# Kernel tuning notes

Measured on AMD Instinct MI355X. Metric: run time of the kernel, lower is better.

Reference implementation:

```python
import jax, jax.numpy as jnp
import numpy as np

B, S, D, H = 8, 2048, 256, 4
HD = D // H  # 64
EPS = 1e-5


def setup_inputs() -> dict:
    key = jax.random.key(0)
    ks = jax.random.split(key, 16)
    sc = 0.05
    return {
        "descriptors": jax.random.normal(ks[0], (B, S, D), jnp.float32),
        "source": jax.random.normal(ks[1], (B, S, D), jnp.float32),
        "mask": jnp.ones((B, S), jnp.int32),
        # attention projections (stored as [in, out])
        "q_w": jax.random.normal(ks[2], (D, D), jnp.float32) * sc,
        "q_b": jnp.zeros((D,), jnp.float32),
        "k_w": jax.random.normal(ks[3], (D, D), jnp.float32) * sc,
        "k_b": jnp.zeros((D,), jnp.float32),
        "v_w": jax.random.normal(ks[4], (D, D), jnp.float32) * sc,
        "v_b": jnp.zeros((D,), jnp.float32),
        "o_w": jax.random.normal(ks[5], (D, D), jnp.float32) * sc,
        "o_b": jnp.zeros((D,), jnp.float32),
        # MLP layer 0: 2D -> 2D, BatchNorm1d (eval mode) + ReLU
        "m0_w": jax.random.normal(ks[6], (2 * D, 2 * D), jnp.float32) * sc,
        "m0_b": jnp.zeros((2 * D,), jnp.float32),
        "bn_g": jax.random.uniform(ks[7], (2 * D,), jnp.float32, 0.5, 1.5),
        "bn_b": jax.random.normal(ks[8], (2 * D,), jnp.float32) * 0.1,
        "bn_m": jax.random.normal(ks[9], (2 * D,), jnp.float32) * 0.1,
        "bn_v": jax.random.uniform(ks[10], (2 * D,), jnp.float32, 0.5, 1.5),
        # MLP layer 1: 2D -> D, no activation
        "m1_w": jax.random.normal(ks[11], (2 * D, D), jnp.float32) * sc,
        "m1_b": jnp.zeros((D,), jnp.float32),
    }


def reference(descriptors, source, mask, q_w, q_b, k_w, k_b, v_w, v_b, o_w, o_b,
              m0_w, m0_b, bn_g, bn_b, bn_m, bn_v, m1_w, m1_b):
    # Multi-head cross-attention: query=descriptors, key=value=source
    q = (descriptors @ q_w + q_b).reshape(B, S, H, HD).transpose(0, 2, 1, 3)  # [B,H,S,HD]
    k = (source @ k_w + k_b).reshape(B, S, H, HD).transpose(0, 2, 1, 3)
    v = (source @ v_w + v_b).reshape(B, S, H, HD).transpose(0, 2, 1, 3)

    scores = jnp.einsum("bhqd,bhkd->bhqk", q, k) / jnp.sqrt(jnp.float32(HD))
    scores = jnp.where(mask[:, None, None, :] == 0, -1e9, scores)
    probs = jax.nn.softmax(scores.astype(jnp.float32), axis=-1)  # [B,H,S,S]

    ctx = jnp.einsum("bhqk,bhkd->bhqd", probs, v)  # [B,H,S,HD]
    ctx = ctx.transpose(0, 2, 1, 3).reshape(B, S, D)
    attn_out = ctx @ o_w + o_b  # out_proj

    # concat + MLP (Linear -> BatchNorm1d(eval) -> ReLU -> Linear)
    h = jnp.concatenate([descriptors, attn_out], axis=-1)  # [B,S,2D]
    h = h @ m0_w + m0_b
    h = (h - bn_m) * jax.lax.rsqrt(bn_v + EPS) * bn_g + bn_b  # per-channel BN
    h = jax.nn.relu(h)
    h = h @ m1_w + m1_b  # [B,S,D]
    return h
```

## Files before the change

kernel.cpp:

```cpp
#include <hip/hip_runtime.h>

#define NB 8
#define NS 2048
#define ND 256
#define NH 4
#define NHD 64
#define ND2 512
#define NM (NB * NS)
#define PITCH 72
#define C1 0.18033688f

typedef __attribute__((ext_vector_type(8))) short          bf16x8;
typedef __attribute__((ext_vector_type(4))) float          f32x4;
typedef unsigned short ushort_t;
typedef unsigned int   uint_t;

#define MFMA16(a, b, c) __builtin_amdgcn_mfma_f32_16x16x32_bf16(a, b, c, 0, 0, 0)

#if __has_builtin(__builtin_amdgcn_exp2f)
#define EXP2(x) __builtin_amdgcn_exp2f(x)
#else
#define EXP2(x) exp2f(x)
#endif

static __device__ inline uint_t pack2bf(float a, float b) {
    union { float f; uint_t u; } x, y; x.f = a; y.f = b;
    return __builtin_amdgcn_perm(y.u + 0x8000u, x.u + 0x8000u, 0x07060302u);
}
static __device__ inline ushort_t f2bf(float f) {
    union { float f; uint_t u; } x; x.f = f;
    return (ushort_t)((x.u + 0x7FFFu + ((x.u >> 16) & 1u)) >> 16);
}


__global__ __launch_bounds__(256) void conv_frag(
    const float* __restrict__ d, const float* __restrict__ s,
    ushort_t* __restrict__ df, ushort_t* __restrict__ sf)
{
    const float* src = blockIdx.y ? s : d;
    ushort_t* dst    = blockIdx.y ? sf : df;
    const int g = blockIdx.x * 256 + threadIdx.x;
    const int lane = g & 63, ci = g >> 6;
    const int kc = ci & 7, r16 = ci >> 3;
    const int row = r16 * 16 + (lane & 15);
    const int c0  = kc * 32 + (lane >> 4) * 8;
    const float* p = src + (size_t)row * ND + c0;
    float4 a = *(const float4*)p;
    float4 b = *(const float4*)(p + 4);
    uint4 pk;
    pk.x = pack2bf(a.x, a.y); pk.y = pack2bf(a.z, a.w);
    pk.z = pack2bf(b.x, b.y); pk.w = pack2bf(b.z, b.w);
    *(uint4*)(dst + (size_t)g * 8) = pk;
}

__global__ __launch_bounds__(256) void wfrag(
    const float* q, const float* k, const float* v, const float* m1,
    ushort_t* qw, ushort_t* kw, ushort_t* vw, ushort_t* m1f)
{
    const float* src; ushort_t* dst; int K, N; float sc = 1.0f;
    switch (blockIdx.y) {
        case 0: src = q;  dst = qw;  K = 256; N = 256; sc = C1; break;
        case 1: src = k;  dst = kw;  K = 256; N = 256; break;
        case 2: src = v;  dst = vw;  K = 256; N = 256; break;
        default: src = m1; dst = m1f; K = 512; N = 256; break;
    }
    const int g = blockIdx.x * 256 + threadIdx.x;
    if (g >= (N * K) / 8) return;
    const int lane = g & 63, ci = g >> 6;
    const int lgck = (K == 512) ? 4 : 3;
    const int kc = ci & ((1 << lgck) - 1), n16 = ci >> lgck;
    const int n  = n16 * 16 + (lane & 15);
    const int k0 = kc * 32 + (lane >> 4) * 8;
    float f[8];
#pragma unroll
    for (int j = 0; j < 8; j++) f[j] = src[(size_t)(k0 + j) * N + n] * sc;
    uint4 pk;
    pk.x = pack2bf(f[0], f[1]); pk.y = pack2bf(f[2], f[3]);
    pk.z = pack2bf(f[4], f[5]); pk.w = pack2bf(f[6], f[7]);
    *(uint4*)(dst + (size_t)g * 8) = pk;
}

static __device__ inline void femit(ushort_t* buf, int n, int k, float v) {
    const int kc = k >> 5;
    const int lane = (((k >> 3) & 3) << 4) | (n & 15);
    const int j = k & 7;
    buf[((size_t)(((n >> 4) * 16 + kc) * 64 + lane)) * 8 + j] = f2bf(v);
}

__global__ __launch_bounds__(256) void fuse_w(
    const float* __restrict__ o_w, const float* __restrict__ o_b,
    const float* __restrict__ m0_w, const float* __restrict__ m0_b,
    const float* __restrict__ bng, const float* __restrict__ bnb,
    const float* __restrict__ bnm, const float* __restrict__ bnv,
    ushort_t* __restrict__ m0fF, float* __restrict__ biasf)
{
    __shared__ float red[256];
    const int n = blockIdx.x;
    const int i = threadIdx.x;
    const float A = bng[n] * rsqrtf(bnv[n] + 1e-5f);
    float f = 0.f;
#pragma unroll 8
    for (int j = 0; j < 256; j++)
        f += o_w[i * 256 + j] * m0_w[(size_t)(256 + j) * 512 + n];
    femit(m0fF, n, 256 + i, f * A);
    femit(m0fF, n, i, m0_w[(size_t)i * 512 + n] * A);
    red[i] = o_b[i] * m0_w[(size_t)(256 + i) * 512 + n];
    __syncthreads();
    for (int s = 128; s > 0; s >>= 1) {
        if (i < s) red[i] += red[i + s];
        __syncthreads();
    }
    if (i == 0) biasf[n] = (m0_b[n] + red[0] - bnm[n]) * A + bnb[n];
}

__global__ __launch_bounds__(256) void make_mbias(
    const int* __restrict__ mask, float* __restrict__ mb)
{
    const int i = blockIdx.x * 256 + threadIdx.x;
    mb[i] = mask[i] ? 0.0f : -1e9f;
}

template <int KC, int AK, bool NAT>
static __device__ inline void core4(
    const ushort_t* __restrict__ A0, const ushort_t* __restrict__ A1,
    const ushort_t* __restrict__ WF, int t16, int n16, f32x4 acc[4][4])
{
    const int lane = threadIdx.x & 63;
#pragma unroll
    for (int kc = 0; kc < KC; kc++) {
        const ushort_t* Ab = (kc < AK) ? A0 : A1;
        const int kca = (kc < AK) ? kc : kc - AK;
        bf16x8 af[4], wf[4];
#pragma unroll
        for (int mt = 0; mt < 4; mt++)
            af[mt] = *(const bf16x8*)(Ab + ((size_t)((t16 + mt) * AK + kca) * 64 + lane) * 8);
#pragma unroll
        for (int nt = 0; nt < 4; nt++)
            wf[nt] = *(const bf16x8*)(WF + ((size_t)((n16 + nt) * KC + kc) * 64 + lane) * 8);
#pragma unroll
        for (int mt = 0; mt < 4; mt++)
#pragma unroll
            for (int nt = 0; nt < 4; nt++) {
                if (NAT) acc[mt][nt] = MFMA16(af[mt], wf[nt], acc[mt][nt]);
                else     acc[mt][nt] = MFMA16(wf[nt], af[mt], acc[mt][nt]);
            }
    }
}

__global__ __launch_bounds__(256) void qkv_frag(
    const ushort_t* __restrict__ descF, const ushort_t* __restrict__ srcF,
    const ushort_t* __restrict__ qwF, const ushort_t* __restrict__ kwF,
    const ushort_t* __restrict__ vwF,
    const float* __restrict__ q_b, const float* __restrict__ k_b,
    const float* __restrict__ v_b,
    ushort_t* __restrict__ qF, ushort_t* __restrict__ kF,
    ushort_t* __restrict__ vF)
{
    const int t = threadIdx.x, w = t >> 6;
    const int lq = t & 15, lg = (t & 63) >> 4;
    const int h    = blockIdx.x;
    const int tok0 = (blockIdx.y << 8) + (w << 6);
    const int t16  = tok0 >> 4, n16 = h << 2;
    const int z    = blockIdx.z;

    f32x4 acc[4][4];
#pragma unroll
    for (int mt = 0; mt < 4; mt++)
#pragma unroll
        for (int nt = 0; nt < 4; nt++) acc[mt][nt] = (f32x4){0.f, 0.f, 0.f, 0.f};

    if (z == 2) {
        core4<8, 8, true>(srcF, srcF, vwF, t16, n16, acc);
#pragma unroll
        for (int nt = 0; nt < 4; nt++) {
            const int dvh = nt * 16 + lq;
            const float bs = v_b[h * 64 + dvh];
#pragma unroll
            for (int mt = 0; mt < 4; mt++) {
                const int tok = tok0 + mt * 16 + lg * 4;
                const int b = tok >> 11, s0 = tok & 2047;
                const int bh = b * NH + h;
                uint2 pv;
                pv.x = pack2bf(acc[mt][nt][0] + bs, acc[mt][nt][1] + bs);
                pv.y = pack2bf(acc[mt][nt][2] + bs, acc[mt][nt][3] + bs);
                const size_t e = (size_t)bh * 131072 +
                    ((size_t)((dvh >> 4) * 64 + (s0 >> 5)) * 64 +
                     (((s0 >> 3) & 3) * 16 + (dvh & 15))) * 8 + (s0 & 7);
                *(uint2*)(vF + e) = pv;
            }
        }
    } else {
        const ushort_t* A = z ? srcF : descF;
        const ushort_t* W = z ? kwF : qwF;
        const float* bias = z ? k_b : q_b;
        ushort_t* dst     = z ? kF : qF;
        const float bsc   = z ? 1.0f : C1;
        core4<8, 8, false>(A, A, W, t16, n16, acc);
#pragma unroll
        for (int nt = 0; nt < 4; nt++) {
            const int d0 = nt * 16 + lg * 4;
            f32x4 b4 = *(const f32x4*)(bias + h * 64 + d0);
#pragma unroll
            for (int mt = 0; mt < 4; mt++) {
                const int tok = tok0 + mt * 16 + lq;
                const int b = tok >> 11, s = tok & 2047;
                const int bh = b * NH + h;
                uint2 pv;
                pv.x = pack2bf(acc[mt][nt][0] + b4[0] * bsc,
                               acc[mt][nt][1] + b4[1] * bsc);
                pv.y = pack2bf(acc[mt][nt][2] + b4[2] * bsc,
                               acc[mt][nt][3] + b4[3] * bsc);
                const size_t e = (size_t)bh * 131072 +
                    ((size_t)((s >> 4) * 2 + (d0 >> 5)) * 64 +
                     (((d0 >> 3) & 3) * 16 + lq)) * 8 + (d0 & 7);
                *(uint2*)(dst + e) = pv;
            }
        }
    }
}

__global__ __launch_bounds__(256) void mlp0_frag(
    const ushort_t* __restrict__ descF, const ushort_t* __restrict__ ctxF,
    const ushort_t* __restrict__ m0fF, const float* __restrict__ biasf,
    ushort_t* __restrict__ hF)
{
    const int t = threadIdx.x, w = t >> 6;
    const int lq = t & 15, lg = (t & 63) >> 4;
    const int n0   = blockIdx.x << 6;
    const int tok0 = (blockIdx.y << 8) + (w << 6);
    const int t16  = tok0 >> 4, n16 = n0 >> 4;

    f32x4 acc[4][4];
#pragma unroll
    for (int mt = 0; mt < 4; mt++)
#pragma unroll
        for (int nt = 0; nt < 4; nt++) acc[mt][nt] = (f32x4){0.f, 0.f, 0.f, 0.f};

    core4<16, 8, false>(descF, ctxF, m0fF, t16, n16, acc);

#pragma unroll
    for (int nt = 0; nt < 4; nt++) {
        const int c0 = n0 + nt * 16 + lg * 4;
        f32x4 b4 = *(const f32x4*)(biasf + c0);
#pragma unroll
        for (int mt = 0; mt < 4; mt++) {
            const int tok = tok0 + mt * 16 + lq;
            uint2 pv;
            pv.x = pack2bf(fmaxf(acc[mt][nt][0] + b4[0], 0.f),
                           fmaxf(acc[mt][nt][1] + b4[1], 0.f));
            pv.y = pack2bf(fmaxf(acc[mt][nt][2] + b4[2], 0.f),
                           fmaxf(acc[mt][nt][3] + b4[3], 0.f));
            const size_t e = ((size_t)((tok >> 4) * 16 + (c0 >> 5)) * 64 +
                              (((c0 >> 3) & 3) * 16 + lq)) * 8 + (c0 & 7);
            *(uint2*)(hF + e) = pv;
        }
    }
}

__global__ __launch_bounds__(256) void mlp1_frag(
    const ushort_t* __restrict__ hF, const ushort_t* __restrict__ m1F,
    const float* __restrict__ m1_b, float* __restrict__ out)
{
    const int t = threadIdx.x, w = t >> 6;
    const int lq = t & 15, lg = (t & 63) >> 4;
    const int n0   = blockIdx.x << 6;
    const int tok0 = (blockIdx.y << 8) + (w << 6);
    const int t16  = tok0 >> 4, n16 = n0 >> 4;

    f32x4 acc[4][4];
#pragma unroll
    for (int mt = 0; mt < 4; mt++)
#pragma unroll
        for (int nt = 0; nt < 4; nt++) acc[mt][nt] = (f32x4){0.f, 0.f, 0.f, 0.f};

    core4<16, 16, false>(hF, hF, m1F, t16, n16, acc);

#pragma unroll
    for (int nt = 0; nt < 4; nt++) {
        const int c0 = n0 + nt * 16 + lg * 4;
        f32x4 b4 = *(const f32x4*)(m1_b + c0);
#pragma unroll
        for (int mt = 0; mt < 4; mt++) {
            const int tok = tok0 + mt * 16 + lq;
            f32x4 o4;
#pragma unroll
            for (int j = 0; j < 4; j++) o4[j] = acc[mt][nt][j] + b4[j];
            *(f32x4*)(out + (size_t)tok * ND + c0) = o4;
        }
    }
}

__global__ __launch_bounds__(256) void attn_frag(
    const ushort_t* __restrict__ qF, const ushort_t* __restrict__ kF,
    const ushort_t* __restrict__ vF, const float* __restrict__ mbias,
    ushort_t* __restrict__ ctxF)
{
    __shared__ ushort_t Pl[8][16 * PITCH];

    const int t = threadIdx.x, w = t >> 6, lane = t & 63;
    const int lq = t & 15, lg = lane >> 4;
    const int qb = blockIdx.x, h = blockIdx.y, b = blockIdx.z;
    const int bh = b * NH + h;

    const ushort_t* qh = qF + (size_t)bh * 131072;
    const ushort_t* kh = kF + (size_t)bh * 131072;
    const ushort_t* vh = vF + (size_t)bh * 131072;
    const float* mrow = mbias + b * NS;
    const int qrow0 = qb * 128 + w * 32;
    const int q16 = qrow0 >> 4;

    bf16x8 qf[2][2];
#pragma unroll
    for (int qt = 0; qt < 2; qt++)
#pragma unroll
        for (int kc = 0; kc < 2; kc++)
            qf[qt][kc] = *(const bf16x8*)(qh + ((size_t)((q16 + qt) * 2 + kc) * 64 + lane) * 8);

    f32x4 o[2][4];
#pragma unroll
    for (int qt = 0; qt < 2; qt++)
#pragma unroll
        for (int dt = 0; dt < 4; dt++) o[qt][dt] = (f32x4){0.f, 0.f, 0.f, 0.f};
    float l_part[2] = {0.0f, 0.0f};

    bf16x8 ka[4][2];
#pragma unroll
    for (int kt = 0; kt < 4; kt++)
#pragma unroll
        for (int kk = 0; kk < 2; kk++)
            ka[kt][kk] = *(const bf16x8*)(kh + ((size_t)((kt * 2 + kk) * 64 + lane)) * 8);

    for (int key0 = 0; key0 < NS; key0 += 64) {
        bf16x8 vf[4][2];
        const ushort_t* vb = vh + (size_t)(key0 >> 5) * 512;
#pragma unroll
        for (int dt = 0; dt < 4; dt++)
#pragma unroll
            for (int kh2 = 0; kh2 < 2; kh2++)
                vf[dt][kh2] = *(const bf16x8*)(vb +
                    ((size_t)((dt * 64 + kh2) * 64 + lane)) * 8);
        f32x4 mb[4];
#pragma unroll
        for (int kt = 0; kt < 4; kt++)
            mb[kt] = *(const f32x4*)(mrow + key0 + kt * 16 + lg * 4);

        f32x4 st[2][4];
#pragma unroll
        for (int qt = 0; qt < 2; qt++)
#pragma unroll
            for (int kt = 0; kt < 4; kt++) {
                f32x4 a = (f32x4){0.f, 0.f, 0.f, 0.f};
                a = MFMA16(ka[kt][0], qf[qt][0], a);
                a = MFMA16(ka[kt][1], qf[qt][1], a);
                st[qt][kt] = a;
            }

        const int keyn = (key0 + 64) & (NS - 1);
        const ushort_t* kb = kh + (size_t)keyn * 64;
        bf16x8 kn[4][2];
#pragma unroll
        for (int kt = 0; kt < 4; kt++)
#pragma unroll
            for (int kk = 0; kk < 2; kk++)
                kn[kt][kk] = *(const bf16x8*)(kb + ((size_t)((kt * 2 + kk) * 64 + lane)) * 8);

#pragma unroll
        for (int qt = 0; qt < 2; qt++) {
            float ls = 0.0f;
#pragma unroll
            for (int kt = 0; kt < 4; kt++) {
                float pr[4];
#pragma unroll
                for (int r = 0; r < 4; r++) {
                    const float p = EXP2(st[qt][kt][r] + mb[kt][r]);
                    ls += p;
                    pr[r] = p;
                }
                uint2 pv;
                pv.x = pack2bf(pr[0], pr[1]);
                pv.y = pack2bf(pr[2], pr[3]);
                *(uint2*)&Pl[w * 2 + qt][lq * PITCH + kt * 16 + lg * 4] = pv;
            }
            l_part[qt] += ls;
        }

        bf16x8 pf[2][2];
#pragma unroll
        for (int qt = 0; qt < 2; qt++)
#pragma unroll
            for (int kh2 = 0; kh2 < 2; kh2++)
                pf[qt][kh2] = *(const bf16x8*)&Pl[w * 2 + qt][lq * PITCH + kh2 * 32 + lg * 8];

#pragma unroll
        for (int dt = 0; dt < 4; dt++)
#pragma unroll
            for (int kh2 = 0; kh2 < 2; kh2++)
#pragma unroll
                for (int qt = 0; qt < 2; qt++)
                    o[qt][dt] = MFMA16(vf[dt][kh2], pf[qt][kh2], o[qt][dt]);

#pragma unroll
        for (int kt = 0; kt < 4; kt++)
#pragma unroll
            for (int kk = 0; kk < 2; kk++)
                ka[kt][kk] = kn[kt][kk];
    }

#pragma unroll
    for (int qt = 0; qt < 2; qt++) {
        float ls = l_part[qt];
        ls += __shfl_xor(ls, 16);
        ls += __shfl_xor(ls, 32);
        const float li = 1.0f / ls;
        const int tok16 = b * 128 + q16 + qt;
#pragma unroll
        for (int dt = 0; dt < 4; dt++) {
            const int c = h * 64 + dt * 16 + lg * 4;
            uint2 pv;
            pv.x = pack2bf(o[qt][dt][0] * li, o[qt][dt][1] * li);
            pv.y = pack2bf(o[qt][dt][2] * li, o[qt][dt][3] * li);
            const size_t e = ((size_t)(tok16 * 8 + (c >> 5)) * 64 +
                              (((c >> 3) & 3) * 16 + lq)) * 8 + (c & 7);
            *(uint2*)(ctxF + e) = pv;
        }
    }
}

extern "C" void kernel_launch(void* const* d_in, const int* in_sizes, int n_in,
                              void* d_out, int out_size, void* d_ws, size_t ws_size,
                              hipStream_t stream)
{
    (void)in_sizes; (void)n_in; (void)out_size; (void)ws_size;
    const float* desc = (const float*)d_in[0];
    const float* srcp = (const float*)d_in[1];
    const int*   mask = (const int*)d_in[2];
    const float* q_w  = (const float*)d_in[3];
    const float* q_b  = (const float*)d_in[4];
    const float* k_w  = (const float*)d_in[5];
    const float* k_b  = (const float*)d_in[6];
    const float* v_w  = (const float*)d_in[7];
    const float* v_b  = (const float*)d_in[8];
    const float* o_w  = (const float*)d_in[9];
    const float* o_b  = (const float*)d_in[10];
    const float* m0_w = (const float*)d_in[11];
    const float* m0_b = (const float*)d_in[12];
    const float* bng  = (const float*)d_in[13];
    const float* bnb  = (const float*)d_in[14];
    const float* bnm  = (const float*)d_in[15];
    const float* bnv  = (const float*)d_in[16];
    const float* m1_w = (const float*)d_in[17];
    const float* m1_b = (const float*)d_in[18];
    float* out = (float*)d_out;

    const size_t ASZ = (size_t)NM * ND;
    ushort_t* descF = (ushort_t*)d_ws;
    ushort_t* srcF  = descF + ASZ;
    ushort_t* qF    = descF + 2 * ASZ;
    ushort_t* kF    = descF + 3 * ASZ;
    ushort_t* vF    = descF + 4 * ASZ;
    ushort_t* qwF   = descF + 5 * ASZ;
    ushort_t* kwF   = qwF + 65536;
    ushort_t* vwF   = kwF + 65536;
    ushort_t* m1F   = vwF + 65536;
    ushort_t* m0fF  = m1F + 131072;
    float*    biasf = (float*)(m0fF + 262144);
    float*    mbias = biasf + 512;
    ushort_t* ctxF  = srcF;
    ushort_t* hF    = qF;

    const dim3 blk(256);

    conv_frag<<<dim3(2048, 2), blk, 0, stream>>>(desc, srcp, descF, srcF);
    wfrag<<<dim3(64, 4), blk, 0, stream>>>(q_w, k_w, v_w, m1_w, qwF, kwF, vwF, m1F);
    fuse_w<<<dim3(512), blk, 0, stream>>>(o_w, o_b, m0_w, m0_b,
                                          bng, bnb, bnm, bnv, m0fF, biasf);
    make_mbias<<<dim3(64), blk, 0, stream>>>(mask, mbias);

    qkv_frag<<<dim3(4, NM / 256, 3), blk, 0, stream>>>(
        descF, srcF, qwF, kwF, vwF, q_b, k_b, v_b, qF, kF, vF);
    attn_frag<<<dim3(NS / 128, NH, NB), blk, 0, stream>>>(qF, kF, vF, mbias, ctxF);
    mlp0_frag<<<dim3(8, NM / 256), blk, 0, stream>>>(descF, ctxF, m0fF, biasf, hF);
    mlp1_frag<<<dim3(4, NM / 256), blk, 0, stream>>>(hF, m1F, m1_b, out);
}
```

Before: 245.2 us.

## Restructure weight fusion, double-buffer GEMM fragments, halve attention block size

```diff
diff --git a/kernel.cpp b/kernel.cpp
--- a/kernel.cpp
+++ b/kernel.cpp
@@ -88,29 +88,44 @@
 }
 
 __global__ __launch_bounds__(256) void fuse_w(
-    const float* __restrict__ o_w, const float* __restrict__ o_b,
-    const float* __restrict__ m0_w, const float* __restrict__ m0_b,
+    const float* __restrict__ o_w, const float* __restrict__ m0_w,
+    const float* __restrict__ bng, const float* __restrict__ bnv,
+    ushort_t* __restrict__ m0fF)
+{
+    __shared__ float ow[256];
+    const int i = blockIdx.x;
+    const int t = threadIdx.x;
+    ow[t] = o_w[i * 256 + t];
+    __syncthreads();
+    float f0 = 0.f, f1 = 0.f;
+#pragma unroll 4
+    for (int j = 0; j < 256; j++) {
+        const float w = ow[j];
+        f0 += w * m0_w[(size_t)(256 + j) * 512 + t];
+        f1 += w * m0_w[(size_t)(256 + j) * 512 + t + 256];
+    }
+    const float A0v = bng[t] * rsqrtf(bnv[t] + 1e-5f);
+    const float A1v = bng[t + 256] * rsqrtf(bnv[t + 256] + 1e-5f);
+    femit(m0fF, t, 256 + i, f0 * A0v);
+    femit(m0fF, t + 256, 256 + i, f1 * A1v);
+    femit(m0fF, t, i, m0_w[(size_t)i * 512 + t] * A0v);
+    femit(m0fF, t + 256, i, m0_w[(size_t)i * 512 + t + 256] * A1v);
+}
+
+__global__ __launch_bounds__(256) void bias_f(
+    const float* __restrict__ o_b, const float* __restrict__ m0_w,
+    const float* __restrict__ m0_b,
     const float* __restrict__ bng, const float* __restrict__ bnb,
     const float* __restrict__ bnm, const float* __restrict__ bnv,
-    ushort_t* __restrict__ m0fF, float* __restrict__ biasf)
-{
-    __shared__ float red[256];
-    const int n = blockIdx.x;
-    const int i = threadIdx.x;
+    float* __restrict__ biasf)
+{
+    const int n = blockIdx.x * 256 + threadIdx.x;
+    float s = 0.f;
+#pragma unroll 4
+    for (int j = 0; j < 256; j++)
+        s += o_b[j] * m0_w[(size_t)(256 + j) * 512 + n];
     const float A = bng[n] * rsqrtf(bnv[n] + 1e-5f);
-    float f = 0.f;
-#pragma unroll 8
-    for (int j = 0; j < 256; j++)
-        f += o_w[i * 256 + j] * m0_w[(size_t)(256 + j) * 512 + n];
-    femit(m0fF, n, 256 + i, f * A);
-    femit(m0fF, n, i, m0_w[(size_t)i * 512 + n] * A);
-    red[i] = o_b[i] * m0_w[(size_t)(256 + i) * 512 + n];
-    __syncthreads();
-    for (int s = 128; s > 0; s >>= 1) {
-        if (i < s) red[i] += red[i + s];
-        __syncthreads();
-    }
-    if (i == 0) biasf[n] = (m0_b[n] + red[0] - bnm[n]) * A + bnb[n];
+    biasf[n] = (m0_b[n] + s - bnm[n]) * A + bnb[n];
 }
 
 __global__ __launch_bounds__(256) void make_mbias(
@@ -126,23 +141,33 @@
     const ushort_t* __restrict__ WF, int t16, int n16, f32x4 acc[4][4])
 {
     const int lane = threadIdx.x & 63;
+    bf16x8 af[2][4], wf[2][4];
+#pragma unroll
+    for (int mt = 0; mt < 4; mt++)
+        af[0][mt] = *(const bf16x8*)(A0 + ((size_t)((t16 + mt) * AK) * 64 + lane) * 8);
+#pragma unroll
+    for (int nt = 0; nt < 4; nt++)
+        wf[0][nt] = *(const bf16x8*)(WF + ((size_t)((n16 + nt) * KC) * 64 + lane) * 8);
 #pragma unroll
     for (int kc = 0; kc < KC; kc++) {
-        const ushort_t* Ab = (kc < AK) ? A0 : A1;
-        const int kca = (kc < AK) ? kc : kc - AK;
-        bf16x8 af[4], wf[4];
+        const int cur = kc & 1, nxt = cur ^ 1;
+        if (kc + 1 < KC) {
+            const int kn = kc + 1;
+            const ushort_t* Ab = (kn < AK) ? A0 : A1;
+            const int kca = (kn < AK) ? kn : kn - AK;
+#pragma unroll
+            for (int mt = 0; mt < 4; mt++)
+                af[nxt][mt] = *(const bf16x8*)(Ab + ((size_t)((t16 + mt) * AK + kca) * 64 + lane) * 8);
+#pragma unroll
+            for (int nt = 0; nt < 4; nt++)
+                wf[nxt][nt] = *(const bf16x8*)(WF + ((size_t)((n16 + nt) * KC + kn) * 64 + lane) * 8);
+        }
 #pragma unroll
         for (int mt = 0; mt < 4; mt++)
-            af[mt] = *(const bf16x8*)(Ab + ((size_t)((t16 + mt) * AK + kca) * 64 + lane) * 8);
-#pragma unroll
-        for (int nt = 0; nt < 4; nt++)
-            wf[nt] = *(const bf16x8*)(WF + ((size_t)((n16 + nt) * KC + kc) * 64 + lane) * 8);
-#pragma unroll
-        for (int mt = 0; mt < 4; mt++)
 #pragma unroll
             for (int nt = 0; nt < 4; nt++) {
-                if (NAT) acc[mt][nt] = MFMA16(af[mt], wf[nt], acc[mt][nt]);
-                else     acc[mt][nt] = MFMA16(wf[nt], af[mt], acc[mt][nt]);
+                if (NAT) acc[mt][nt] = MFMA16(af[cur][mt], wf[cur][nt], acc[mt][nt]);
+                else     acc[mt][nt] = MFMA16(wf[cur][nt], af[cur][mt], acc[mt][nt]);
             }
     }
 }
@@ -290,12 +315,12 @@
     }
 }
 
-__global__ __launch_bounds__(256) void attn_frag(
+__global__ __launch_bounds__(128) void attn_frag(
     const ushort_t* __restrict__ qF, const ushort_t* __restrict__ kF,
     const ushort_t* __restrict__ vF, const float* __restrict__ mbias,
     ushort_t* __restrict__ ctxF)
 {
-    __shared__ ushort_t Pl[8][16 * PITCH];
+    __shared__ ushort_t Pl[4][16 * PITCH];
 
     const int t = threadIdx.x, w = t >> 6, lane = t & 63;
     const int lq = t & 15, lg = lane >> 4;
@@ -306,7 +331,7 @@
     const ushort_t* kh = kF + (size_t)bh * 131072;
     const ushort_t* vh = vF + (size_t)bh * 131072;
     const float* mrow = mbias + b * NS;
-    const int qrow0 = qb * 128 + w * 32;
+    const int qrow0 = qb * 64 + w * 32;
     const int q16 = qrow0 >> 4;
 
     bf16x8 qf[2][2];
@@ -472,13 +497,13 @@
 
     conv_frag<<<dim3(2048, 2), blk, 0, stream>>>(desc, srcp, descF, srcF);
     wfrag<<<dim3(64, 4), blk, 0, stream>>>(q_w, k_w, v_w, m1_w, qwF, kwF, vwF, m1F);
-    fuse_w<<<dim3(512), blk, 0, stream>>>(o_w, o_b, m0_w, m0_b,
-                                          bng, bnb, bnm, bnv, m0fF, biasf);
+    fuse_w<<<dim3(256), blk, 0, stream>>>(o_w, m0_w, bng, bnv, m0fF);
+    bias_f<<<dim3(2), blk, 0, stream>>>(o_b, m0_w, m0_b, bng, bnb, bnm, bnv, biasf);
     make_mbias<<<dim3(64), blk, 0, stream>>>(mask, mbias);
 
     qkv_frag<<<dim3(4, NM / 256, 3), blk, 0, stream>>>(
         descF, srcF, qwF, kwF, vwF, q_b, k_b, v_b, qF, kF, vF);
-    attn_frag<<<dim3(NS / 128, NH, NB), blk, 0, stream>>>(qF, kF, vF, mbias, ctxF);
+    attn_frag<<<dim3(NS / 64, NH, NB), dim3(128), 0, stream>>>(qF, kF, vF, mbias, ctxF);
     mlp0_frag<<<dim3(8, NM / 256), blk, 0, stream>>>(descF, ctxF, m0fF, biasf, hF);
     mlp1_frag<<<dim3(4, NM / 256), blk, 0, stream>>>(hF, m1F, m1_b, out);
 }
```

New measurement: 269.3 us. +9.8%, slower.

## Merge prep kernels, restructure fuse_w, remap attention blocks, shrink mlp1 tiles

Applied to the files above, without the earlier changes.

```diff
diff --git a/kernel.cpp b/kernel.cpp
--- a/kernel.cpp
+++ b/kernel.cpp
@@ -33,53 +33,6 @@
 }
 
 
-__global__ __launch_bounds__(256) void conv_frag(
-    const float* __restrict__ d, const float* __restrict__ s,
-    ushort_t* __restrict__ df, ushort_t* __restrict__ sf)
-{
-    const float* src = blockIdx.y ? s : d;
-    ushort_t* dst    = blockIdx.y ? sf : df;
-    const int g = blockIdx.x * 256 + threadIdx.x;
-    const int lane = g & 63, ci = g >> 6;
-    const int kc = ci & 7, r16 = ci >> 3;
-    const int row = r16 * 16 + (lane & 15);
-    const int c0  = kc * 32 + (lane >> 4) * 8;
-    const float* p = src + (size_t)row * ND + c0;
-    float4 a = *(const float4*)p;
-    float4 b = *(const float4*)(p + 4);
-    uint4 pk;
-    pk.x = pack2bf(a.x, a.y); pk.y = pack2bf(a.z, a.w);
-    pk.z = pack2bf(b.x, b.y); pk.w = pack2bf(b.z, b.w);
-    *(uint4*)(dst + (size_t)g * 8) = pk;
-}
-
-__global__ __launch_bounds__(256) void wfrag(
-    const float* q, const float* k, const float* v, const float* m1,
-    ushort_t* qw, ushort_t* kw, ushort_t* vw, ushort_t* m1f)
-{
-    const float* src; ushort_t* dst; int K, N; float sc = 1.0f;
-    switch (blockIdx.y) {
-        case 0: src = q;  dst = qw;  K = 256; N = 256; sc = C1; break;
-        case 1: src = k;  dst = kw;  K = 256; N = 256; break;
-        case 2: src = v;  dst = vw;  K = 256; N = 256; break;
-        default: src = m1; dst = m1f; K = 512; N = 256; break;
-    }
-    const int g = blockIdx.x * 256 + threadIdx.x;
-    if (g >= (N * K) / 8) return;
-    const int lane = g & 63, ci = g >> 6;
-    const int lgck = (K == 512) ? 4 : 3;
-    const int kc = ci & ((1 << lgck) - 1), n16 = ci >> lgck;
-    const int n  = n16 * 16 + (lane & 15);
-    const int k0 = kc * 32 + (lane >> 4) * 8;
-    float f[8];
-#pragma unroll
-    for (int j = 0; j < 8; j++) f[j] = src[(size_t)(k0 + j) * N + n] * sc;
-    uint4 pk;
-    pk.x = pack2bf(f[0], f[1]); pk.y = pack2bf(f[2], f[3]);
-    pk.z = pack2bf(f[4], f[5]); pk.w = pack2bf(f[6], f[7]);
-    *(uint4*)(dst + (size_t)g * 8) = pk;
-}
-
 static __device__ inline void femit(ushort_t* buf, int n, int k, float v) {
     const int kc = k >> 5;
     const int lane = (((k >> 3) & 3) << 4) | (n & 15);
@@ -87,58 +40,122 @@
     buf[((size_t)(((n >> 4) * 16 + kc) * 64 + lane)) * 8 + j] = f2bf(v);
 }
 
-__global__ __launch_bounds__(256) void fuse_w(
+__global__ __launch_bounds__(256) void prep(
+    const float* __restrict__ desc, const float* __restrict__ srcp,
+    const int* __restrict__ mask,
+    const float* __restrict__ q_w, const float* __restrict__ k_w,
+    const float* __restrict__ v_w, const float* __restrict__ m1_w,
     const float* __restrict__ o_w, const float* __restrict__ o_b,
     const float* __restrict__ m0_w, const float* __restrict__ m0_b,
     const float* __restrict__ bng, const float* __restrict__ bnb,
     const float* __restrict__ bnm, const float* __restrict__ bnv,
-    ushort_t* __restrict__ m0fF, float* __restrict__ biasf)
-{
-    __shared__ float red[256];
-    const int n = blockIdx.x;
-    const int i = threadIdx.x;
-    const float A = bng[n] * rsqrtf(bnv[n] + 1e-5f);
-    float f = 0.f;
-#pragma unroll 8
-    for (int j = 0; j < 256; j++)
-        f += o_w[i * 256 + j] * m0_w[(size_t)(256 + j) * 512 + n];
-    femit(m0fF, n, 256 + i, f * A);
-    femit(m0fF, n, i, m0_w[(size_t)i * 512 + n] * A);
-    red[i] = o_b[i] * m0_w[(size_t)(256 + i) * 512 + n];
-    __syncthreads();
-    for (int s = 128; s > 0; s >>= 1) {
-        if (i < s) red[i] += red[i + s];
+    ushort_t* __restrict__ descF, ushort_t* __restrict__ srcF,
+    ushort_t* __restrict__ qwF, ushort_t* __restrict__ kwF,
+    ushort_t* __restrict__ vwF, ushort_t* __restrict__ m1F,
+    ushort_t* __restrict__ m0fF, float* __restrict__ biasf,
+    float* __restrict__ mbias)
+{
+    __shared__ float ow[256];
+    const int blk = blockIdx.x;
+    const int t = threadIdx.x;
+
+    if (blk < 4096) {
+        const int y = blk >> 11, x = blk & 2047;
+        const float* src = y ? srcp : desc;
+        ushort_t* dst    = y ? srcF : descF;
+        const int g = x * 256 + t;
+        const int lane = g & 63, ci = g >> 6;
+        const int kc = ci & 7, r16 = ci >> 3;
+        const int row = r16 * 16 + (lane & 15);
+        const int c0  = kc * 32 + (lane >> 4) * 8;
+        const float* p = src + (size_t)row * ND + c0;
+        float4 a = *(const float4*)p;
+        float4 b = *(const float4*)(p + 4);
+        uint4 pk;
+        pk.x = pack2bf(a.x, a.y); pk.y = pack2bf(a.z, a.w);
+        pk.z = pack2bf(b.x, b.y); pk.w = pack2bf(b.z, b.w);
+        *(uint4*)(dst + (size_t)g * 8) = pk;
+    } else if (blk < 4352) {
+        const int wb = blk - 4096;
+        const int y = wb >> 6, x = wb & 63;
+        const float* src; ushort_t* dst; int K, N; float sc = 1.0f;
+        switch (y) {
+            case 0: src = q_w; dst = qwF; K = 256; N = 256; sc = C1; break;
+            case 1: src = k_w; dst = kwF; K = 256; N = 256; break;
+            case 2: src = v_w; dst = vwF; K = 256; N = 256; break;
+            default: src = m1_w; dst = m1F; K = 512; N = 256; break;
+        }
+        const int g = x * 256 + t;
+        if (g >= (N * K) / 8) return;
+        const int lane = g & 63, ci = g >> 6;
+        const int lgck = (K == 512) ? 4 : 3;
+        const int kc = ci & ((1 << lgck) - 1), n16 = ci >> lgck;
+        const int n  = n16 * 16 + (lane & 15);
+        const int k0 = kc * 32 + (lane >> 4) * 8;
+        float f[8];
+#pragma unroll
+        for (int j = 0; j < 8; j++) f[j] = src[(size_t)(k0 + j) * N + n] * sc;
+        uint4 pk;
+        pk.x = pack2bf(f[0], f[1]); pk.y = pack2bf(f[2], f[3]);
+        pk.z = pack2bf(f[4], f[5]); pk.w = pack2bf(f[6], f[7]);
+        *(uint4*)(dst + (size_t)g * 8) = pk;
+    } else if (blk < 4416) {
+        const int i = (blk - 4352) * 256 + t;
+        mbias[i] = mask[i] ? 0.0f : -1e9f;
+    } else if (blk < 4672) {
+        const int i = blk - 4416;
+        ow[t] = o_w[i * 256 + t];
         __syncthreads();
-    }
-    if (i == 0) biasf[n] = (m0_b[n] + red[0] - bnm[n]) * A + bnb[n];
-}
-
-__global__ __launch_bounds__(256) void make_mbias(
-    const int* __restrict__ mask, float* __restrict__ mb)
-{
-    const int i = blockIdx.x * 256 + threadIdx.x;
-    mb[i] = mask[i] ? 0.0f : -1e9f;
-}
-
-template <int KC, int AK, bool NAT>
-static __device__ inline void core4(
+        float f0 = 0.f, f1 = 0.f;
+#pragma unroll 4
+        for (int j = 0; j < 256; j++) {
+            const float w = ow[j];
+            f0 += w * m0_w[(size_t)(256 + j) * 512 + t];
+            f1 += w * m0_w[(size_t)(256 + j) * 512 + t + 256];
+        }
+        const float A0v = bng[t] * rsqrtf(bnv[t] + 1e-5f);
+        const float A1v = bng[t + 256] * rsqrtf(bnv[t + 256] + 1e-5f);
+        femit(m0fF, t, 256 + i, f0 * A0v);
+        femit(m0fF, t + 256, 256 + i, f1 * A1v);
+        femit(m0fF, t, i, m0_w[(size_t)i * 512 + t] * A0v);
+        femit(m0fF, t + 256, i, m0_w[(size_t)i * 512 + t + 256] * A1v);
+    } else {
+        const int bb = blk - 4672;
+        const int n  = bb * 32 + (t >> 3);
+        const int jp = t & 7;
+        float s = 0.f;
+#pragma unroll 4
+        for (int j = jp * 32; j < jp * 32 + 32; j++)
+            s += o_b[j] * m0_w[(size_t)(256 + j) * 512 + n];
+        s += __shfl_xor(s, 1);
+        s += __shfl_xor(s, 2);
+        s += __shfl_xor(s, 4);
+        if (jp == 0) {
+            const float A = bng[n] * rsqrtf(bnv[n] + 1e-5f);
+            biasf[n] = (m0_b[n] + s - bnm[n]) * A + bnb[n];
+        }
+    }
+}
+
+template <int KC, int AK, bool NAT, int MT>
+static __device__ inline void core(
     const ushort_t* __restrict__ A0, const ushort_t* __restrict__ A1,
-    const ushort_t* __restrict__ WF, int t16, int n16, f32x4 acc[4][4])
+    const ushort_t* __restrict__ WF, int t16, int n16, f32x4 acc[MT][4])
 {
     const int lane = threadIdx.x & 63;
 #pragma unroll
     for (int kc = 0; kc < KC; kc++) {
         const ushort_t* Ab = (kc < AK) ? A0 : A1;
         const int kca = (kc < AK) ? kc : kc - AK;
-        bf16x8 af[4], wf[4];
-#pragma unroll
-        for (int mt = 0; mt < 4; mt++)
+        bf16x8 af[MT], wf[4];
+#pragma unroll
+        for (int mt = 0; mt < MT; mt++)
             af[mt] = *(const bf16x8*)(Ab + ((size_t)((t16 + mt) * AK + kca) * 64 + lane) * 8);
 #pragma unroll
         for (int nt = 0; nt < 4; nt++)
             wf[nt] = *(const bf16x8*)(WF + ((size_t)((n16 + nt) * KC + kc) * 64 + lane) * 8);
 #pragma unroll
-        for (int mt = 0; mt < 4; mt++)
+        for (int mt = 0; mt < MT; mt++)
 #pragma unroll
             for (int nt = 0; nt < 4; nt++) {
                 if (NAT) acc[mt][nt] = MFMA16(af[mt], wf[nt], acc[mt][nt]);
@@ -170,7 +187,7 @@
         for (int nt = 0; nt < 4; nt++) acc[mt][nt] = (f32x4){0.f, 0.f, 0.f, 0.f};
 
     if (z == 2) {
-        core4<8, 8, true>(srcF, srcF, vwF, t16, n16, acc);
+        core<8, 8, true, 4>(srcF, srcF, vwF, t16, n16, acc);
 #pragma unroll
         for (int nt = 0; nt < 4; nt++) {
             const int dvh = nt * 16 + lq;
@@ -195,7 +212,7 @@
         const float* bias = z ? k_b : q_b;
         ushort_t* dst     = z ? kF : qF;
         const float bsc   = z ? 1.0f : C1;
-        core4<8, 8, false>(A, A, W, t16, n16, acc);
+        core<8, 8, false, 4>(A, A, W, t16, n16, acc);
 #pragma unroll
         for (int nt = 0; nt < 4; nt++) {
             const int d0 = nt * 16 + lg * 4;
@@ -236,7 +253,7 @@
 #pragma unroll
         for (int nt = 0; nt < 4; nt++) acc[mt][nt] = (f32x4){0.f, 0.f, 0.f, 0.f};
 
-    core4<16, 8, false>(descF, ctxF, m0fF, t16, n16, acc);
+    core<16, 8, false, 4>(descF, ctxF, m0fF, t16, n16, acc);
 
 #pragma unroll
     for (int nt = 0; nt < 4; nt++) {
@@ -264,23 +281,23 @@
     const int t = threadIdx.x, w = t >> 6;
     const int lq = t & 15, lg = (t & 63) >> 4;
     const int n0   = blockIdx.x << 6;
-    const int tok0 = (blockIdx.y << 8) + (w << 6);
+    const int tok0 = (blockIdx.y << 7) + (w << 5);
     const int t16  = tok0 >> 4, n16 = n0 >> 4;
 
-    f32x4 acc[4][4];
-#pragma unroll
-    for (int mt = 0; mt < 4; mt++)
+    f32x4 acc[2][4];
+#pragma unroll
+    for (int mt = 0; mt < 2; mt++)
 #pragma unroll
         for (int nt = 0; nt < 4; nt++) acc[mt][nt] = (f32x4){0.f, 0.f, 0.f, 0.f};
 
-    core4<16, 16, false>(hF, hF, m1F, t16, n16, acc);
+    core<16, 16, false, 2>(hF, hF, m1F, t16, n16, acc);
 
 #pragma unroll
     for (int nt = 0; nt < 4; nt++) {
         const int c0 = n0 + nt * 16 + lg * 4;
         f32x4 b4 = *(const f32x4*)(m1_b + c0);
 #pragma unroll
-        for (int mt = 0; mt < 4; mt++) {
+        for (int mt = 0; mt < 2; mt++) {
             const int tok = tok0 + mt * 16 + lq;
             f32x4 o4;
 #pragma unroll
@@ -299,13 +316,16 @@
 
     const int t = threadIdx.x, w = t >> 6, lane = t & 63;
     const int lq = t & 15, lg = lane >> 4;
-    const int qb = blockIdx.x, h = blockIdx.y, b = blockIdx.z;
-    const int bh = b * NH + h;
+    const int flat = blockIdx.x + (blockIdx.y << 4) + (blockIdx.z << 6);
+    const int bh = (flat & 7) + (((flat >> 7) & 3) << 3);
+    const int qb = (flat >> 3) & 15;
+    const int b = bh >> 2, h = bh & 3;
+    (void)b; (void)h;
 
     const ushort_t* qh = qF + (size_t)bh * 131072;
     const ushort_t* kh = kF + (size_t)bh * 131072;
     const ushort_t* vh = vF + (size_t)bh * 131072;
-    const float* mrow = mbias + b * NS;
+    const float* mrow = mbias + (bh >> 2) * NS;
     const int qrow0 = qb * 128 + w * 32;
     const int q16 = qrow0 >> 4;
 
@@ -412,10 +432,10 @@
         ls += __shfl_xor(ls, 16);
         ls += __shfl_xor(ls, 32);
         const float li = 1.0f / ls;
-        const int tok16 = b * 128 + q16 + qt;
+        const int tok16 = (bh >> 2) * 128 + q16 + qt;
 #pragma unroll
         for (int dt = 0; dt < 4; dt++) {
-            const int c = h * 64 + dt * 16 + lg * 4;
+            const int c = (bh & 3) * 64 + dt * 16 + lg * 4;
             uint2 pv;
             pv.x = pack2bf(o[qt][dt][0] * li, o[qt][dt][1] * li);
             pv.y = pack2bf(o[qt][dt][2] * li, o[qt][dt][3] * li);
@@ -470,15 +490,13 @@
 
     const dim3 blk(256);
 
-    conv_frag<<<dim3(2048, 2), blk, 0, stream>>>(desc, srcp, descF, srcF);
-    wfrag<<<dim3(64, 4), blk, 0, stream>>>(q_w, k_w, v_w, m1_w, qwF, kwF, vwF, m1F);
-    fuse_w<<<dim3(512), blk, 0, stream>>>(o_w, o_b, m0_w, m0_b,
-                                          bng, bnb, bnm, bnv, m0fF, biasf);
-    make_mbias<<<dim3(64), blk, 0, stream>>>(mask, mbias);
+    prep<<<dim3(4688), blk, 0, stream>>>(
+        desc, srcp, mask, q_w, k_w, v_w, m1_w, o_w, o_b, m0_w, m0_b,
+        bng, bnb, bnm, bnv, descF, srcF, qwF, kwF, vwF, m1F, m0fF, biasf, mbias);
 
     qkv_frag<<<dim3(4, NM / 256, 3), blk, 0, stream>>>(
         descF, srcF, qwF, kwF, vwF, q_b, k_b, v_b, qF, kF, vF);
     attn_frag<<<dim3(NS / 128, NH, NB), blk, 0, stream>>>(qF, kF, vF, mbias, ctxF);
     mlp0_frag<<<dim3(8, NM / 256), blk, 0, stream>>>(descF, ctxF, m0fF, biasf, hF);
-    mlp1_frag<<<dim3(4, NM / 256), blk, 0, stream>>>(hF, m1F, m1_b, out);
-}
+    mlp1_frag<<<dim3(4, NM / 128), blk, 0, stream>>>(hF, m1F, m1_b, out);
+}
```

After: 239.8 us. 2.2% less time.
